# Optimization experiments

Measured on AMD Instinct MI355X. Metric: run time of the kernel, lower is better.

Reference implementation:

```python
import math
import jax, jax.numpy as jnp
from jax import lax
import numpy as np

SIGMA_SCALES = [0.6 * 2 ** i for i in range(6)]  # [0.6, 1.2, 2.4, 4.8, 9.6, 19.2]


def _gauss1d(sigma: float, ks: int) -> np.ndarray:
    # ax = arange(-ks//2+1, ks//2+1) for odd ks == arange(ks) - ks//2 (symmetric)
    ax = np.arange(ks, dtype=np.float32) - ks // 2
    k = np.exp(-(ax ** 2) / (2.0 * sigma ** 2))
    return (k / k.sum()).astype(np.float32)


def _kernel_size(sigma: float) -> int:
    return max(7, 2 * math.ceil(3.0 * sigma) + 1)


def _gaussian_blur(img, sigma):
    # Separable depthwise Gaussian: the torch module's 2D kernel
    # exp(-(x^2+y^2)/2s^2)/Z factors exactly into outer(g1, g1) of normalized 1D kernels.
    B, C, H, W = img.shape
    ks = _kernel_size(sigma)
    p = ks // 2
    g1 = jnp.asarray(_gauss1d(sigma, ks), dtype=img.dtype)
    x = jnp.pad(img, ((0, 0), (0, 0), (p, p), (p, p)), mode='reflect')
    kh = jnp.broadcast_to(g1.reshape(1, 1, ks, 1), (C, 1, ks, 1))
    kw = jnp.broadcast_to(g1.reshape(1, 1, 1, ks), (C, 1, 1, ks))
    dn = ('NCHW', 'OIHW', 'NCHW')
    x = lax.conv_general_dilated(x, kh, (1, 1), 'VALID', dimension_numbers=dn,
                                 feature_group_count=C)
    x = lax.conv_general_dilated(x, kw, (1, 1), 'VALID', dimension_numbers=dn,
                                 feature_group_count=C)
    return x  # (B, C, H, W)


def setup_inputs() -> dict:
    key = jax.random.key(0)
    img = jax.random.normal(key, (8, 3, 512, 512), dtype=jnp.float32)
    return {"img": img}


def reference(img) -> jnp.ndarray:
    # gaussians = [img, G(s0)*img, G(s1)*img, ...]; each scale filters the ORIGINAL img.
    gaussians = [img]
    for sigma in SIGMA_SCALES:
        gaussians.append(_gaussian_blur(img, sigma))
    n = len(gaussians)
    subbands = [gaussians[i + 1] - gaussians[i] for i in range(n - 1)]
    subbands.append(gaussians[-1])
    return jnp.stack(subbands, axis=1)  # (B, len(scales)+1, C, H, W)
```

## Files before the change

### kernel.cpp

```cpp
#include <hip/hip_runtime.h>
#include <cmath>
#include <cstddef>

#define BATCH 8
#define CH    3
#define HH    512
#define WW    512
#define NSLOT 7
#define HWX   (HH*WW)

#define NWP 352
struct WP { float w[NWP]; };

__device__ __host__ __forceinline__ int refl(int i, int n) {
    i = i < 0 ? -i : i;
    return i >= n ? 2 * n - 2 - i : i;
}

template<int KS> struct WArr { float w[KS + 16]; };

constexpr double cexp_(double x) {
    double r = x / 64.0, term = 1.0, s = 1.0;
    for (int i = 1; i < 26; ++i) { term *= r / i; s += term; }
    for (int j = 0; j < 6; ++j) s *= s;
    return s;
}

template<int KS>
constexpr WArr<KS> make_w(double sg) {
    WArr<KS> a{};
    double tmp[KS] = {};
    double sum = 0.0;
    for (int t = 0; t < KS; ++t) {
        const double ax = (double)(t - KS / 2);
        tmp[t] = cexp_(-(ax * ax) / (2.0 * sg * sg));
        sum += tmp[t];
    }
    for (int i = 0; i < KS + 16; ++i) a.w[i] = 0.0f;
    for (int t = 0; t < KS; ++t) a.w[8 + t] = (float)(tmp[t] / sum);
    return a;
}

__device__ constexpr WArr<7>   CW0 = make_w<7>(0.6);
__device__ constexpr WArr<9>   CW1 = make_w<9>(1.2);
__device__ constexpr WArr<17>  CW2 = make_w<17>(2.4);
__device__ constexpr WArr<31>  CW3 = make_w<31>(4.8);
__device__ constexpr WArr<59>  CW4 = make_w<59>(9.6);
__device__ constexpr WArr<117> CW5 = make_w<117>(19.2);

template<int KS, int PD, int WOP>
__device__ __forceinline__ void vpass16(const float4* __restrict__ img4,
                                        float4* __restrict__ dst,
                                        int xt, int y0, const WP& wp)
{
    float4 acc[16];
#pragma unroll
    for (int j = 0; j < 16; ++j) acc[j] = make_float4(0.f, 0.f, 0.f, 0.f);
#pragma unroll 2
    for (int t = 0; t < KS + 15; ++t) {
        const int yi = refl(y0 - PD + t, HH);
        const float4 v = img4[(size_t)yi * (WW / 4) + xt];
#pragma unroll
        for (int j = 0; j < 16; ++j) {
            const float wt = wp.w[WOP + t - j];
            acc[j].x = fmaf(wt, v.x, acc[j].x);
            acc[j].y = fmaf(wt, v.y, acc[j].y);
            acc[j].z = fmaf(wt, v.z, acc[j].z);
            acc[j].w = fmaf(wt, v.w, acc[j].w);
        }
    }
#pragma unroll
    for (int j = 0; j < 16; ++j) dst[(size_t)(y0 + j) * (WW / 4) + xt] = acc[j];
}

__global__ __launch_bounds__(128) void vpass6_kernel(const float* __restrict__ img,
                                                     float* __restrict__ out, WP wp)
{
    const int s  = blockIdx.x;
    const int xt = threadIdx.x;
    const int y0 = blockIdx.y * 16;
    const int bc = blockIdx.z;
    const int b = bc / CH, c = bc - b * CH;
    const float4* img4 = (const float4*)img + (size_t)bc * (HWX / 4);
    float4* dst = (float4*)out + ((size_t)((b * NSLOT + s + 1) * CH) + c) * (HWX / 4);
    switch (s) {
        case 0: vpass16<  7,  3,  16>(img4, dst, xt, y0, wp); break;
        case 1: vpass16<  9,  4,  39>(img4, dst, xt, y0, wp); break;
        case 2: vpass16< 17,  8,  64>(img4, dst, xt, y0, wp); break;
        case 3: vpass16< 31, 15,  97>(img4, dst, xt, y0, wp); break;
        case 4: vpass16< 59, 29, 144>(img4, dst, xt, y0, wp); break;
        default:vpass16<117, 58, 219>(img4, dst, xt, y0, wp); break;
    }
}

template<int KS>
__device__ __forceinline__ float4 hblur4c(const float* __restrict__ lrow, int xt,
                                          const WArr<KS>& W)
{
    constexpr int NT = (KS + 3) & ~3;
    const float4* l4 = (const float4*)lrow;
    float cb[16];
    {
        float4 t0 = l4[xt + 0];
        cb[0] = t0.x; cb[1] = t0.y; cb[2] = t0.z; cb[3] = t0.w;
        float4 t1 = l4[xt + 1];
        cb[4] = t1.x; cb[5] = t1.y; cb[6] = t1.z; cb[7] = t1.w;
    }
    float a[4] = {0.f, 0.f, 0.f, 0.f};
#pragma unroll
    for (int tb = 0; tb < NT; tb += 4) {
        const int ls = ((tb >> 2) + 2) & 3;
        float4 tn = l4[xt + (tb >> 2) + 2];
        cb[ls * 4 + 0] = tn.x; cb[ls * 4 + 1] = tn.y;
        cb[ls * 4 + 2] = tn.z; cb[ls * 4 + 3] = tn.w;
#pragma unroll
        for (int tt = 0; tt < 4; ++tt) {
            const float wt = W.w[8 + tb + tt];
#pragma unroll
            for (int j = 0; j < 4; ++j) {
                const int q    = tt + j;
                const int slot = ((tb >> 2) + (q >> 2)) & 3;
                a[j] = fmaf(wt, cb[slot * 4 + (q & 3)], a[j]);
            }
        }
    }
    return make_float4(a[0], a[1], a[2], a[3]);
}

#define LDSROW 3860

template<int OFF, int LEN, int PD>
__device__ __forceinline__ void stage_row(float* __restrict__ L,
                                          const float* __restrict__ g, int xt)
{
    for (int i = xt; i < LEN; i += 128) L[OFF + i] = g[refl(i - PD, WW)];
}

__device__ __forceinline__ float4 f4sub(float4 a, float4 b) {
    return make_float4(a.x - b.x, a.y - b.y, a.z - b.z, a.w - b.w);
}

__global__ __launch_bounds__(256) void hdiff6_kernel(const float* __restrict__ img,
                                                     float* __restrict__ out)
{
    __shared__ __align__(16) float lds[2][LDSROW];
    const int xt = threadIdx.x;
    const int r  = threadIdx.y;
    const int y  = blockIdx.y * 2 + r;
    const int bc = blockIdx.z;
    const int b = bc / CH, c = bc - b * CH;
    float* L = lds[r];

    const float* irow = img + ((size_t)bc * HH + y) * WW;
    ((float4*)L)[xt] = ((const float4*)irow)[xt];

    const size_t rowoff = (size_t)y * WW;
    const float* g1 = out + ((size_t)((b * NSLOT + 1) * CH) + c) * HWX + rowoff;
    const float* g2 = out + ((size_t)((b * NSLOT + 2) * CH) + c) * HWX + rowoff;
    const float* g3 = out + ((size_t)((b * NSLOT + 3) * CH) + c) * HWX + rowoff;
    const float* g4 = out + ((size_t)((b * NSLOT + 4) * CH) + c) * HWX + rowoff;
    const float* g5 = out + ((size_t)((b * NSLOT + 5) * CH) + c) * HWX + rowoff;
    const float* g6 = out + ((size_t)((b * NSLOT + 6) * CH) + c) * HWX + rowoff;
    stage_row< 512, 524,  3>(L, g1, xt);
    stage_row<1036, 528,  4>(L, g2, xt);
    stage_row<1564, 536,  8>(L, g3, xt);
    stage_row<2100, 548, 15>(L, g4, xt);
    stage_row<2648, 576, 29>(L, g5, xt);
    stage_row<3224, 636, 58>(L, g6, xt);
    __syncthreads();

    float4* out4 = (float4*)out;
    const size_t pbase = (size_t)y * (WW / 4) + xt;
#define OSL(s) (out4 + ((size_t)((b * NSLOT + (s)) * CH) + c) * (HWX / 4) + pbase)

    float4 gp = ((const float4*)L)[xt];
    float4 g;
    g = hblur4c<  7>(L +  512, xt, CW0); *OSL(0) = f4sub(g, gp); gp = g;
    g = hblur4c<  9>(L + 1036, xt, CW1); *OSL(1) = f4sub(g, gp); gp = g;
    g = hblur4c< 17>(L + 1564, xt, CW2); *OSL(2) = f4sub(g, gp); gp = g;
    g = hblur4c< 31>(L + 2100, xt, CW3); *OSL(3) = f4sub(g, gp); gp = g;
    g = hblur4c< 59>(L + 2648, xt, CW4); *OSL(4) = f4sub(g, gp); gp = g;
    g = hblur4c<117>(L + 3224, xt, CW5); *OSL(5) = f4sub(g, gp);
    *OSL(6) = g;
#undef OSL
}

static void fill_wp(WP& wp)
{
    const double sig[6] = {0.6, 1.2, 2.4, 4.8, 9.6, 19.2};
    const int ks[6]  = {7, 9, 17, 31, 59, 117};
    const int wop[6] = {16, 39, 64, 97, 144, 219};
    for (int i = 0; i < NWP; ++i) wp.w[i] = 0.f;
    for (int s = 0; s < 6; ++s) {
        const int k = ks[s], p = k / 2;
        double sum = 0.0;
        for (int t = 0; t < k; ++t) {
            const double ax = (double)(t - p);
            const double v = std::exp(-(ax * ax) / (2.0 * sig[s] * sig[s]));
            wp.w[wop[s] + t] = (float)v;
            sum += v;
        }
        const float inv = (float)(1.0 / sum);
        for (int t = 0; t < k; ++t) wp.w[wop[s] + t] *= inv;
    }
}

extern "C" void kernel_launch(void* const* d_in, const int* in_sizes, int n_in,
                              void* d_out, int out_size, void* d_ws, size_t ws_size,
                              hipStream_t stream) {
    const float* img = (const float*)d_in[0];
    float* out = (float*)d_out;

    WP wp;
    fill_wp(wp);

    const dim3 bv(128, 1), gv(6, HH / 16, BATCH * CH);
    hipLaunchKernelGGL(vpass6_kernel, gv, bv, 0, stream, img, out, wp);

    const dim3 bh(128, 2), gh(1, HH / 2, BATCH * CH);
    hipLaunchKernelGGL(hdiff6_kernel, gh, bh, 0, stream, img, out);
}
```

Baseline: 391.5 us.

## Block vertical pass into 16-tap chunks with register-rotated constexpr weights

The vertical blur loop now walks taps in blocks of 16. Weights come from per-scale constexpr device arrays and are held in two rotating register windows, replacing indexed loads from a kernel-argument struct. The horizontal kernel stages each row with float4 loads plus a separate reflect fill for the borders, and reads the original image straight from global memory instead of through LDS, which shrinks the LDS row buffer. The risks are higher register pressure from the 16-entry weight windows and extra zero-padded taps in the vertical pass.

```diff
diff --git a/kernel.cpp b/kernel.cpp
--- a/kernel.cpp
+++ b/kernel.cpp
@@ -9,15 +9,10 @@
 #define NSLOT 7
 #define HWX   (HH*WW)
 
-#define NWP 352
-struct WP { float w[NWP]; };
-
 __device__ __host__ __forceinline__ int refl(int i, int n) {
     i = i < 0 ? -i : i;
     return i >= n ? 2 * n - 2 - i : i;
 }
-
-template<int KS> struct WArr { float w[KS + 16]; };
 
 constexpr double cexp_(double x) {
     double r = x / 64.0, term = 1.0, s = 1.0;
@@ -25,6 +20,8 @@
     for (int j = 0; j < 6; ++j) s *= s;
     return s;
 }
+
+template<int KS> struct WArr { float w[KS + 16]; };
 
 template<int KS>
 constexpr WArr<KS> make_w(double sg) {
@@ -48,33 +45,75 @@
 __device__ constexpr WArr<59>  CW4 = make_w<59>(9.6);
 __device__ constexpr WArr<117> CW5 = make_w<117>(19.2);
 
-template<int KS, int PD, int WOP>
+template<int KS> struct VWArr {
+    static constexpr int TPAD = (KS + 30) & ~15;
+    float w[TPAD + 16];
+};
+
+template<int KS>
+constexpr VWArr<KS> make_vw(double sg) {
+    VWArr<KS> a{};
+    double tmp[KS] = {};
+    double sum = 0.0;
+    for (int t = 0; t < KS; ++t) {
+        const double ax = (double)(t - KS / 2);
+        tmp[t] = cexp_(-(ax * ax) / (2.0 * sg * sg));
+        sum += tmp[t];
+    }
+    for (int i = 0; i < VWArr<KS>::TPAD + 16; ++i) a.w[i] = 0.0f;
+    for (int t = 0; t < KS; ++t) a.w[16 + t] = (float)(tmp[t] / sum);
+    return a;
+}
+
+__device__ constexpr VWArr<7>   VW0 = make_vw<7>(0.6);
+__device__ constexpr VWArr<9>   VW1 = make_vw<9>(1.2);
+__device__ constexpr VWArr<17>  VW2 = make_vw<17>(2.4);
+__device__ constexpr VWArr<31>  VW3 = make_vw<31>(4.8);
+__device__ constexpr VWArr<59>  VW4 = make_vw<59>(9.6);
+__device__ constexpr VWArr<117> VW5 = make_vw<117>(19.2);
+
+template<int KS, int PD>
 __device__ __forceinline__ void vpass16(const float4* __restrict__ img4,
                                         float4* __restrict__ dst,
-                                        int xt, int y0, const WP& wp)
-{
+                                        int xt, int y0, const float* __restrict__ vw)
+{
+    constexpr int TPAD = (KS + 30) & ~15;
     float4 acc[16];
 #pragma unroll
     for (int j = 0; j < 16; ++j) acc[j] = make_float4(0.f, 0.f, 0.f, 0.f);
-#pragma unroll 2
-    for (int t = 0; t < KS + 15; ++t) {
-        const int yi = refl(y0 - PD + t, HH);
-        const float4 v = img4[(size_t)yi * (WW / 4) + xt];
-#pragma unroll
-        for (int j = 0; j < 16; ++j) {
-            const float wt = wp.w[WOP + t - j];
-            acc[j].x = fmaf(wt, v.x, acc[j].x);
-            acc[j].y = fmaf(wt, v.y, acc[j].y);
-            acc[j].z = fmaf(wt, v.z, acc[j].z);
-            acc[j].w = fmaf(wt, v.w, acc[j].w);
+
+    float ww[16];
+#pragma unroll
+    for (int m = 0; m < 16; ++m) ww[m] = vw[m];
+
+#pragma unroll 1
+    for (int tb = 0; tb < TPAD; tb += 16) {
+        float wn[16];
+#pragma unroll
+        for (int k = 0; k < 16; ++k) wn[k] = vw[tb + 16 + k];
+#pragma unroll
+        for (int k = 0; k < 16; ++k) {
+            const int yi = refl(y0 - PD + tb + k, HH);
+            const float4 v = img4[(size_t)yi * (WW / 4) + xt];
+#pragma unroll
+            for (int j = 0; j < 16; ++j) {
+                const int mi = 16 + k - j;
+                const float wt = (mi < 16) ? ww[mi] : wn[mi - 16];
+                acc[j].x = fmaf(wt, v.x, acc[j].x);
+                acc[j].y = fmaf(wt, v.y, acc[j].y);
+                acc[j].z = fmaf(wt, v.z, acc[j].z);
+                acc[j].w = fmaf(wt, v.w, acc[j].w);
+            }
         }
+#pragma unroll
+        for (int m = 0; m < 16; ++m) ww[m] = wn[m];
     }
 #pragma unroll
     for (int j = 0; j < 16; ++j) dst[(size_t)(y0 + j) * (WW / 4) + xt] = acc[j];
 }
 
 __global__ __launch_bounds__(128) void vpass6_kernel(const float* __restrict__ img,
-                                                     float* __restrict__ out, WP wp)
+                                                     float* __restrict__ out)
 {
     const int s  = blockIdx.x;
     const int xt = threadIdx.x;
@@ -84,12 +123,12 @@
     const float4* img4 = (const float4*)img + (size_t)bc * (HWX / 4);
     float4* dst = (float4*)out + ((size_t)((b * NSLOT + s + 1) * CH) + c) * (HWX / 4);
     switch (s) {
-        case 0: vpass16<  7,  3,  16>(img4, dst, xt, y0, wp); break;
-        case 1: vpass16<  9,  4,  39>(img4, dst, xt, y0, wp); break;
-        case 2: vpass16< 17,  8,  64>(img4, dst, xt, y0, wp); break;
-        case 3: vpass16< 31, 15,  97>(img4, dst, xt, y0, wp); break;
-        case 4: vpass16< 59, 29, 144>(img4, dst, xt, y0, wp); break;
-        default:vpass16<117, 58, 219>(img4, dst, xt, y0, wp); break;
+        case 0: vpass16<  7,  3>(img4, dst, xt, y0, VW0.w); break;
+        case 1: vpass16<  9,  4>(img4, dst, xt, y0, VW1.w); break;
+        case 2: vpass16< 17,  8>(img4, dst, xt, y0, VW2.w); break;
+        case 3: vpass16< 31, 15>(img4, dst, xt, y0, VW3.w); break;
+        case 4: vpass16< 59, 29>(img4, dst, xt, y0, VW4.w); break;
+        default:vpass16<117, 58>(img4, dst, xt, y0, VW5.w); break;
     }
 }
 
@@ -127,13 +166,22 @@
     return make_float4(a[0], a[1], a[2], a[3]);
 }
 
-#define LDSROW 3860
+#define LDSROW 3348
 
 template<int OFF, int LEN, int PD>
 __device__ __forceinline__ void stage_row(float* __restrict__ L,
                                           const float* __restrict__ g, int xt)
 {
-    for (int i = xt; i < LEN; i += 128) L[OFF + i] = g[refl(i - PD, WW)];
+    const float4 v = ((const float4*)g)[xt];
+    if constexpr ((PD & 3) == 0) {
+        ((float4*)(L + OFF + PD))[xt] = v;
+    } else {
+        float* d = L + OFF + PD + 4 * xt;
+        d[0] = v.x; d[1] = v.y; d[2] = v.z; d[3] = v.w;
+    }
+    if (xt < PD) L[OFF + xt] = g[PD - xt];
+    for (int i = PD + 512 + xt; i < LEN; i += 128)
+        L[OFF + i] = g[2 * WW - 2 - (i - PD)];
 }
 
 __device__ __forceinline__ float4 f4sub(float4 a, float4 b) {
@@ -151,58 +199,31 @@
     const int b = bc / CH, c = bc - b * CH;
     float* L = lds[r];
 
-    const float* irow = img + ((size_t)bc * HH + y) * WW;
-    ((float4*)L)[xt] = ((const float4*)irow)[xt];
-
     const size_t rowoff = (size_t)y * WW;
+    constexpr size_t SSTR = (size_t)CH * HWX;
     const float* g1 = out + ((size_t)((b * NSLOT + 1) * CH) + c) * HWX + rowoff;
-    const float* g2 = out + ((size_t)((b * NSLOT + 2) * CH) + c) * HWX + rowoff;
-    const float* g3 = out + ((size_t)((b * NSLOT + 3) * CH) + c) * HWX + rowoff;
-    const float* g4 = out + ((size_t)((b * NSLOT + 4) * CH) + c) * HWX + rowoff;
-    const float* g5 = out + ((size_t)((b * NSLOT + 5) * CH) + c) * HWX + rowoff;
-    const float* g6 = out + ((size_t)((b * NSLOT + 6) * CH) + c) * HWX + rowoff;
-    stage_row< 512, 524,  3>(L, g1, xt);
-    stage_row<1036, 528,  4>(L, g2, xt);
-    stage_row<1564, 536,  8>(L, g3, xt);
-    stage_row<2100, 548, 15>(L, g4, xt);
-    stage_row<2648, 576, 29>(L, g5, xt);
-    stage_row<3224, 636, 58>(L, g6, xt);
+    stage_row<   0, 524,  3>(L, g1,            xt);
+    stage_row< 524, 528,  4>(L, g1 + 1 * SSTR, xt);
+    stage_row<1052, 536,  8>(L, g1 + 2 * SSTR, xt);
+    stage_row<1588, 548, 15>(L, g1 + 3 * SSTR, xt);
+    stage_row<2136, 576, 29>(L, g1 + 4 * SSTR, xt);
+    stage_row<2712, 636, 58>(L, g1 + 5 * SSTR, xt);
     __syncthreads();
 
     float4* out4 = (float4*)out;
     const size_t pbase = (size_t)y * (WW / 4) + xt;
 #define OSL(s) (out4 + ((size_t)((b * NSLOT + (s)) * CH) + c) * (HWX / 4) + pbase)
 
-    float4 gp = ((const float4*)L)[xt];
+    float4 gp = ((const float4*)(img + (size_t)bc * HWX + rowoff))[xt];
     float4 g;
-    g = hblur4c<  7>(L +  512, xt, CW0); *OSL(0) = f4sub(g, gp); gp = g;
-    g = hblur4c<  9>(L + 1036, xt, CW1); *OSL(1) = f4sub(g, gp); gp = g;
-    g = hblur4c< 17>(L + 1564, xt, CW2); *OSL(2) = f4sub(g, gp); gp = g;
-    g = hblur4c< 31>(L + 2100, xt, CW3); *OSL(3) = f4sub(g, gp); gp = g;
-    g = hblur4c< 59>(L + 2648, xt, CW4); *OSL(4) = f4sub(g, gp); gp = g;
-    g = hblur4c<117>(L + 3224, xt, CW5); *OSL(5) = f4sub(g, gp);
+    g = hblur4c<  7>(L +    0, xt, CW0); *OSL(0) = f4sub(g, gp); gp = g;
+    g = hblur4c<  9>(L +  524, xt, CW1); *OSL(1) = f4sub(g, gp); gp = g;
+    g = hblur4c< 17>(L + 1052, xt, CW2); *OSL(2) = f4sub(g, gp); gp = g;
+    g = hblur4c< 31>(L + 1588, xt, CW3); *OSL(3) = f4sub(g, gp); gp = g;
+    g = hblur4c< 59>(L + 2136, xt, CW4); *OSL(4) = f4sub(g, gp); gp = g;
+    g = hblur4c<117>(L + 2712, xt, CW5); *OSL(5) = f4sub(g, gp);
     *OSL(6) = g;
 #undef OSL
-}
-
-static void fill_wp(WP& wp)
-{
-    const double sig[6] = {0.6, 1.2, 2.4, 4.8, 9.6, 19.2};
-    const int ks[6]  = {7, 9, 17, 31, 59, 117};
-    const int wop[6] = {16, 39, 64, 97, 144, 219};
-    for (int i = 0; i < NWP; ++i) wp.w[i] = 0.f;
-    for (int s = 0; s < 6; ++s) {
-        const int k = ks[s], p = k / 2;
-        double sum = 0.0;
-        for (int t = 0; t < k; ++t) {
-            const double ax = (double)(t - p);
-            const double v = std::exp(-(ax * ax) / (2.0 * sig[s] * sig[s]));
-            wp.w[wop[s] + t] = (float)v;
-            sum += v;
-        }
-        const float inv = (float)(1.0 / sum);
-        for (int t = 0; t < k; ++t) wp.w[wop[s] + t] *= inv;
-    }
 }
 
 extern "C" void kernel_launch(void* const* d_in, const int* in_sizes, int n_in,
@@ -211,11 +232,8 @@
     const float* img = (const float*)d_in[0];
     float* out = (float*)d_out;
 
-    WP wp;
-    fill_wp(wp);
-
     const dim3 bv(128, 1), gv(6, HH / 16, BATCH * CH);
-    hipLaunchKernelGGL(vpass6_kernel, gv, bv, 0, stream, img, out, wp);
+    hipLaunchKernelGGL(vpass6_kernel, gv, bv, 0, stream, img, out);
 
     const dim3 bh(128, 2), gh(1, HH / 2, BATCH * CH);
     hipLaunchKernelGGL(hdiff6_kernel, gh, bh, 0, stream, img, out);
```

Result: faster. 381.4 us (-2.6%).
